# Optimization experiments

Hardware: AMD Instinct MI355X
Metric: run time of the kernel (lower is better)

The kernel has to match this reference:

```python
import jax, jax.numpy as jnp
import numpy as np

B, N, IN, HD, NH, L, OUT = 256, 128, 9, 128, 8, 4, 60
DH = HD // NH
ALPHA = 0.6
EPS = 1e-5

def _ln(x, g, b):
    m = jnp.mean(x, axis=-1, keepdims=True)
    v = jnp.mean((x - m) ** 2, axis=-1, keepdims=True)
    return (x - m) * jax.lax.rsqrt(v + EPS) * g + b

def setup_inputs():
    key = jax.random.key(0)
    ks = jax.random.split(key, 30)
    p = lambda i, s: jax.random.normal(ks[i], s, jnp.float32) * 0.02
    strong = (jax.random.uniform(ks[25], (N, N)) < 0.15).astype(jnp.float32)
    strong = jnp.maximum(strong, jnp.eye(N, dtype=jnp.float32))  # self loops
    weak_mask = (jax.random.uniform(ks[26], (N, N)) < 0.10).astype(jnp.float32)
    return {
        'x': jax.random.normal(ks[0], (B, N, IN), jnp.float32),
        'conv_w': p(1, (HD, IN)), 'conv_b': p(2, (HD,)),
        'bn_gamma': jnp.ones((HD,), jnp.float32), 'bn_beta': jnp.zeros((HD,), jnp.float32),
        'bn_mean': jnp.zeros((HD,), jnp.float32), 'bn_var': jnp.ones((HD,), jnp.float32),
        'W': p(3, (L, HD, HD)), 'a_src': p(4, (L, NH, DH)), 'a_dst': p(5, (L, NH, DH)),
        'ln_g': jnp.ones((L, HD), jnp.float32), 'ln_b': jnp.zeros((L, HD), jnp.float32),
        'ffn_w1': p(6, (L, HD, 2 * HD)), 'ffn_b1': p(7, (L, 2 * HD)),
        'ffn_w2': p(8, (L, 2 * HD, HD)), 'ffn_b2': p(9, (L, HD)),
        'norm_g': jnp.ones((HD,), jnp.float32), 'norm_b': jnp.zeros((HD,), jnp.float32),
        'proj_w': p(10, (HD, HD)), 'proj_b': p(11, (HD,)),
        'head_w1': p(12, (HD, HD // 2)), 'head_b1': p(13, (HD // 2,)),
        'head_w2': p(14, (HD // 2, OUT)), 'head_b2': p(15, (OUT,)),
        'strong_adj': strong, 'weak_mask': weak_mask,
        'weak_param': p(16, (N, N)), 'edge_weight_adj': p(17, (N, N)),
    }

def reference(x, conv_w, conv_b, bn_gamma, bn_beta, bn_mean, bn_var, W, a_src, a_dst, ln_g, ln_b, ffn_w1, ffn_b1, ffn_w2, ffn_b2, norm_g, norm_b, proj_w, proj_b, head_w1, head_b1, head_w2, head_b2, strong_adj, weak_mask, weak_param, edge_weight_adj):
    # embedding: Conv1d(k=1) == per-node linear, then eval-mode BatchNorm1d + ReLU
    h = jnp.einsum('bni,oi->bno', x, conv_w) + conv_b  # [B,N,HD]
    h = (h - bn_mean) * jax.lax.rsqrt(bn_var + EPS) * bn_gamma + bn_beta
    h = jax.nn.relu(h)
    # weak adjacency: learnable gated edges, row-normalized (shared across layers)
    Aw = jax.nn.sigmoid(weak_param) * weak_mask
    Aw = Aw / (jnp.sum(Aw, axis=-1, keepdims=True) + EPS)  # [N,N]
    for i in range(L):
        res = h
        hp = jnp.einsum('bnd,de->bne', h, W[i]).reshape(B, N, NH, DH)
        s = jnp.einsum('bnhd,hd->bnh', hp, a_src[i])
        t = jnp.einsum('bnhd,hd->bnh', hp, a_dst[i])
        e = jax.nn.leaky_relu(s[:, :, None, :] + t[:, None, :, :], 0.2)  # [B,N,N,H]
        e = e + edge_weight_adj[None, :, :, None]  # learned per-edge bias
        e = jnp.where(strong_adj[None, :, :, None] > 0, e, jnp.float32(-1e9))
        att = jax.nn.softmax(e, axis=2)  # softmax over neighbors j
        strong_out = jnp.einsum('bijh,bjhd->bihd', att, hp)
        weak_out = jnp.einsum('ij,bjhd->bihd', Aw, hp)
        g = jax.nn.relu(ALPHA * strong_out + (1.0 - ALPHA) * weak_out).reshape(B, N, HD)
        g = _ln(g, ln_g[i], ln_b[i])
        g = jax.nn.relu(g @ ffn_w1[i] + ffn_b1[i]) @ ffn_w2[i] + ffn_b2[i]
        h = g + res
    h = _ln(h, norm_g, norm_b)
    h = h @ proj_w + proj_b
    h = jnp.mean(h, axis=1)  # mean-pool over nodes -> [B,HD]
    h = jax.nn.relu(h @ head_w1 + head_b1)
    return h @ head_w2 + head_b2  # [B,OUT]
```

## Files before the change

### kernel.cpp

```cpp
#include <hip/hip_runtime.h>
#include <hip/hip_bf16.h>

typedef __hip_bfloat16 bf16;
typedef unsigned short u16;
typedef __attribute__((ext_vector_type(8))) short bfrag;
typedef __attribute__((ext_vector_type(4))) float cfrag;

union BF { bfrag v; u16 u[8]; unsigned w[4]; };
union CF { cfrag v; float f[4]; };

#define MFMA(a,b,c) __builtin_amdgcn_mfma_f32_16x16x32_bf16(a,b,c,0,0,0)

#define BB   256
#define NN   128
#define IND  9
#define HDD  128
#define NHH  8
#define LLY  4
#define OUTD 60
#define LOG2E 1.44269504f

__device__ __forceinline__ float b2f(bf16 v){ return __bfloat162float(v); }
__device__ __forceinline__ float u2f(u16 u){ return __uint_as_float(((unsigned)u) << 16); }
__device__ __forceinline__ u16 f2bf_bits(float f){
    unsigned u = __float_as_uint(f);
    return (u16)((u + 0x7FFFu + ((u >> 16) & 1u)) >> 16);
}
__device__ __forceinline__ unsigned pk2(float a, float b){
    union { __hip_bfloat162 h; unsigned u; } c;
    c.h = __float22bfloat162_rn(make_float2(a, b));
    return c.u;
}
__device__ __forceinline__ float wave_sum(float v){
    #pragma unroll
    for (int m = 32; m; m >>= 1) v += __shfl_xor(v, m, 64);
    return v;
}
__device__ __forceinline__ float ldin(const void* p, int i, bool isbf){
    return isbf ? b2f(((const bf16*)p)[i]) : ((const float*)p)[i];
}

struct SrcPtrs { const void* p[28]; };

__device__ const int CVT_OFF[28] = {
    0,294912,296064,296192,296320,296448,296576,296704,362240,362752,363264,363776,
    364288,495360,496384,627456,627968,628096,628224,644608,644736,652928,652992,656832,
    656896,673280,689664,706048};

__global__ __launch_bounds__(256) void k_prep(
    SrcPtrs S, float* __restrict__ pf,
    u16* __restrict__ WT, u16* __restrict__ w1T, u16* __restrict__ w2T,
    u16* __restrict__ ew2, u16* __restrict__ Aw16, int* __restrict__ flagOut)
{
    const unsigned* xw = (const unsigned*)S.p[0];
    int lane = threadIdx.x & 63;
    int cnt = 0;
    for (int i = lane; i < 512; i += 64) {
        float v = __uint_as_float((xw[i] & 0xFFFFu) << 16);
        if (!(fabsf(v) < 32.f)) cnt++;
    }
    bool isbf = wave_sum((float)cnt) < 16.f;
    if (blockIdx.x == 0 && threadIdx.x == 0) *flagOut = isbf ? 1 : 0;

    int blk = blockIdx.x, tid = threadIdx.x;
    if (blk < 2822) {
        int idx = blk * 256 + tid;
        int y = 27;
        #pragma unroll 1
        for (int t = 1; t < 28; t++) if (idx < CVT_OFF[t]) { y = t - 1; break; }
        pf[idx] = ldin(S.p[y], idx - CVT_OFF[y], isbf);
    } else if (blk < 3078) {
        int j = (blk - 2822) * 256 + tid;
        int l = j >> 14, r = j & 16383, n = r >> 7, k = r & 127;
        WT[j] = f2bf_bits(ldin(S.p[7], (l << 14) + k * 128 + n, isbf));
    } else if (blk < 3590) {
        int j = (blk - 3078) * 256 + tid;
        int l = j >> 15, r = j & 32767, n = r >> 7, k = r & 127;
        w1T[j] = f2bf_bits(ldin(S.p[12], (l << 15) + k * 256 + n, isbf));
    } else if (blk < 4102) {
        int j = (blk - 3590) * 256 + tid;
        int l = j >> 15, r = j & 32767, n = r >> 8, k = r & 255;
        w2T[j] = f2bf_bits(ldin(S.p[14], (l << 15) + k * 128 + n, isbf));
    } else if (blk < 4166) {
        int j = (blk - 4102) * 256 + tid;
        float sav = ldin(S.p[24], j, isbf);
        float ewv = ldin(S.p[27], j, isbf);
        ew2[j] = f2bf_bits(sav > 0.f ? ewv * LOG2E : -1e30f);
    } else {
        __shared__ float red[2];
        int i = blk - 4166, j = tid & 127;
        float v = 0.f;
        if (tid < 128) {
            float wmv = ldin(S.p[25], i * 128 + j, isbf);
            float wpv = ldin(S.p[26], i * 128 + j, isbf);
            v = wmv / (1.f + __expf(-wpv));
            float sm = wave_sum(v);
            if ((tid & 63) == 0) red[tid >> 6] = sm;
        }
        __syncthreads();
        if (tid < 128) {
            float tot = red[0] + red[1];
            Aw16[i * 128 + j] = f2bf_bits(v / (tot + 1e-5f));
        }
    }
}

__global__ __launch_bounds__(256) void k_embed(
    const float* __restrict__ xf, const float* __restrict__ cw, const float* __restrict__ cb,
    const float* __restrict__ bg, const float* __restrict__ bbt,
    const float* __restrict__ bm, const float* __restrict__ bv,
    float* __restrict__ h, u16* __restrict__ h16)
{
    int b = blockIdx.x, half = blockIdx.y, tid = threadIdx.x;
    int d = tid & 127, nh = tid >> 7;
    float wreg[IND];
    #pragma unroll
    for (int k = 0; k < IND; k++) wreg[k] = cw[d * IND + k];
    float scale = rsqrtf(bv[d] + 1e-5f) * bg[d];
    float bias  = bbt[d] - bm[d] * scale;
    float cbd   = cb[d];
    #pragma unroll 1
    for (int it = 0; it < 32; it++) {
        int bn = b * NN + half * 64 + it * 2 + nh;
        float acc = cbd;
        #pragma unroll
        for (int k = 0; k < IND; k++) acc = fmaf(xf[bn * IND + k], wreg[k], acc);
        acc = fmaxf(fmaf(acc, scale, bias), 0.f);
        h[bn * HDD + d] = acc;
        h16[bn * HDD + d] = f2bf_bits(acc);
    }
}

__global__ __launch_bounds__(256, 2) void k_layer(
    float* __restrict__ hg, u16* __restrict__ h16g,
    const u16* __restrict__ WT,
    const float* __restrict__ asrc, const float* __restrict__ adst,
    const u16* __restrict__ Aw16, const u16* __restrict__ ew2g,
    const float* __restrict__ lng, const float* __restrict__ lnb,
    const u16* __restrict__ w1T, const float* __restrict__ b1,
    const u16* __restrict__ w2T, const float* __restrict__ b2,
    const float* __restrict__ ng, const float* __restrict__ nb,
    float* __restrict__ pooled, int last)
{
    __shared__ __align__(16) u16 hpT[128 * 136];
    __shared__ __align__(16) u16 gbuf[64 * 136];
    __shared__ float st2[2048];
    __shared__ float lng_s[128], lnb_s[128], b2_s[128], ng_s[128], nb_s[128];
    __shared__ float b1_s[256];
    u16* hidb = hpT;
    float* s2 = st2;
    float* t2 = st2 + 1024;

    const int b = blockIdx.x, half = blockIdx.y;
    const int tid = threadIdx.x, lane = tid & 63, wv = tid >> 6;
    const int l15 = lane & 15, kg = lane >> 4;
    const int wrow = wv * 16;
    const int base = b * NN;

    if (tid < 128) {
        lng_s[tid] = lng[tid]; lnb_s[tid] = lnb[tid]; b2_s[tid] = b2[tid];
        if (last) { ng_s[tid] = ng[tid]; nb_s[tid] = nb[tid]; }
    }
    b1_s[tid] = b1[tid];

    {
        CF acc[2][8];
        #pragma unroll
        for (int mt = 0; mt < 2; mt++)
            #pragma unroll
            for (int nt = 0; nt < 8; nt++)
                #pragma unroll
                for (int r = 0; r < 4; r++) acc[mt][nt].f[r] = 0.f;
        #pragma unroll 1
        for (int kk = 0; kk < 4; kk++) {
            bfrag af0 = *(const bfrag*)&h16g[(base + wv*32 +      l15) * 128 + kk*32 + kg*8];
            bfrag af1 = *(const bfrag*)&h16g[(base + wv*32 + 16 + l15) * 128 + kk*32 + kg*8];
            #pragma unroll
            for (int nt = 0; nt < 8; nt++) {
                bfrag bw = *(const bfrag*)&WT[(nt*16 + l15) * 128 + kk*32 + kg*8];
                acc[0][nt].v = MFMA(af0, bw, acc[0][nt].v);
                acc[1][nt].v = MFMA(af1, bw, acc[1][nt].v);
            }
        }
        #pragma unroll
        for (int mt = 0; mt < 2; mt++)
            #pragma unroll
            for (int nt = 0; nt < 8; nt++) {
                int col = nt*16 + l15;
                #pragma unroll
                for (int rp = 0; rp < 2; rp++) {
                    int row = wv*32 + mt*16 + kg*4 + rp*2;
                    *(unsigned*)&hpT[col * 136 + row] =
                        pk2(acc[mt][nt].f[rp*2], acc[mt][nt].f[rp*2+1]);
                }
            }
    }
    __syncthreads();

    {
        int node = tid & 127, which = tid >> 7;
        const float* av = which ? adst : asrc;
        float* dst = which ? t2 : s2;
        #pragma unroll 1
        for (int h = 0; h < 8; h++) {
            const u16* cp = &hpT[h * 16 * 136 + node];
            float a = 0.f;
            #pragma unroll
            for (int d = 0; d < 16; d++)
                a = fmaf(u2f(cp[d * 136]), av[h*16 + d], a);
            dst[h * 128 + node] = a * LOG2E;
        }
    }
    __syncthreads();

    CF accS[8];
    #pragma unroll
    for (int nt = 0; nt < 8; nt++)
        #pragma unroll
        for (int r = 0; r < 4; r++) accS[nt].f[r] = 0.f;

    const int grow = half*64 + wrow + l15;
    #pragma unroll 1
    for (int h = 0; h < 8; h++) {
        bfrag hb[4];
        #pragma unroll
        for (int kk = 0; kk < 4; kk++)
            hb[kk] = *(const bfrag*)&hpT[(h*16 + l15) * 136 + kk*32 + kg*8];
        float sA = s2[h * 128 + grow];
        float pv[4][8];
        float sm = 0.f;
        #pragma unroll
        for (int kk = 0; kk < 4; kk++) {
            const float* tp = &t2[h * 128 + kk*32 + kg*8];
            BF e2; e2.v = *(const bfrag*)&ew2g[grow * 128 + kk*32 + kg*8];
            #pragma unroll
            for (int j = 0; j < 8; j++) {
                float x2 = sA + tp[j];
                float lk = fmaxf(x2, 0.2f * x2);
                float p = __builtin_amdgcn_exp2f(lk + u2f(e2.u[j]));
                pv[kk][j] = p; sm += p;
            }
        }
        sm += __shfl_xor(sm, 16, 64);
        sm += __shfl_xor(sm, 32, 64);
        float inv = __builtin_amdgcn_rcpf(sm);
        #pragma unroll
        for (int kk = 0; kk < 4; kk++) {
            BF pb;
            #pragma unroll
            for (int q = 0; q < 4; q++)
                pb.w[q] = pk2(pv[kk][2*q] * inv, pv[kk][2*q+1] * inv);
            accS[h].v = MFMA(pb.v, hb[kk], accS[h].v);
        }
    }

    CF accW[8];
    #pragma unroll
    for (int nt = 0; nt < 8; nt++)
        #pragma unroll
        for (int r = 0; r < 4; r++) accW[nt].f[r] = 0.f;
    #pragma unroll 1
    for (int kk = 0; kk < 4; kk++) {
        bfrag awf = *(const bfrag*)&Aw16[grow * 128 + kk*32 + kg*8];
        #pragma unroll
        for (int nt = 0; nt < 8; nt++) {
            bfrag hb2 = *(const bfrag*)&hpT[(nt*16 + l15) * 136 + kk*32 + kg*8];
            accW[nt].v = MFMA(awf, hb2, accW[nt].v);
        }
    }

    {
        float gv[8][4];
        #pragma unroll
        for (int nt = 0; nt < 8; nt++)
            #pragma unroll
            for (int r = 0; r < 4; r++)
                gv[nt][r] = fmaxf(0.6f * accS[nt].f[r] + 0.4f * accW[nt].f[r], 0.f);
        #pragma unroll
        for (int r = 0; r < 4; r++) {
            float s1 = 0.f, sq = 0.f;
            #pragma unroll
            for (int nt = 0; nt < 8; nt++) { float x = gv[nt][r]; s1 += x; sq = fmaf(x, x, sq); }
            #pragma unroll
            for (int m = 1; m <= 8; m <<= 1) { s1 += __shfl_xor(s1, m, 64); sq += __shfl_xor(sq, m, 64); }
            float mu = s1 * (1.f / 128.f);
            float var = sq * (1.f / 128.f) - mu * mu;
            float rs = rsqrtf(fmaxf(var, 0.f) + 1e-5f);
            int lrow = wrow + kg*4 + r;
            #pragma unroll
            for (int nt = 0; nt < 8; nt++) {
                int col = nt*16 + l15;
                gbuf[lrow * 136 + col] = f2bf_bits(fmaf((gv[nt][r] - mu) * rs, lng_s[col], lnb_s[col]));
            }
        }
    }
    __syncthreads();

    CF acc2[8];
    #pragma unroll
    for (int nt = 0; nt < 8; nt++)
        #pragma unroll
        for (int r = 0; r < 4; r++) acc2[nt].f[r] = 0.f;

    #pragma unroll 1
    for (int nh = 0; nh < 2; nh++) {
        CF a1[8];
        #pragma unroll
        for (int nt = 0; nt < 8; nt++)
            #pragma unroll
            for (int r = 0; r < 4; r++) a1[nt].f[r] = 0.f;
        #pragma unroll 1
        for (int kk = 0; kk < 4; kk++) {
            bfrag gf = *(const bfrag*)&gbuf[(wrow + l15) * 136 + kk*32 + kg*8];
            #pragma unroll
            for (int nt = 0; nt < 8; nt++) {
                bfrag wf = *(const bfrag*)&w1T[(nh*128 + nt*16 + l15) * 128 + kk*32 + kg*8];
                a1[nt].v = MFMA(gf, wf, a1[nt].v);
            }
        }
        __syncthreads();
        #pragma unroll
        for (int nt = 0; nt < 8; nt++) {
            int col = nt*16 + l15;
            #pragma unroll
            for (int r = 0; r < 4; r++) {
                int lrow = wrow + kg*4 + r;
                hidb[lrow * 136 + col] = f2bf_bits(fmaxf(a1[nt].f[r] + b1_s[nh*128 + col], 0.f));
            }
        }
        __syncthreads();
        #pragma unroll 1
        for (int kk = 0; kk < 4; kk++) {
            bfrag hf = *(const bfrag*)&hidb[(wrow + l15) * 136 + kk*32 + kg*8];
            #pragma unroll
            for (int nt = 0; nt < 8; nt++) {
                bfrag wf = *(const bfrag*)&w2T[(nt*16 + l15) * 256 + nh*128 + kk*32 + kg*8];
                acc2[nt].v = MFMA(hf, wf, acc2[nt].v);
            }
        }
    }

    float hv[8][4];
    #pragma unroll
    for (int nt = 0; nt < 8; nt++) {
        int col = nt*16 + l15;
        #pragma unroll
        for (int r = 0; r < 4; r++) {
            int gi = (base + half*64 + wrow + kg*4 + r) * HDD + col;
            hv[nt][r] = acc2[nt].f[r] + b2_s[col] + hg[gi];
        }
    }
    if (!last) {
        #pragma unroll
        for (int nt = 0; nt < 8; nt++) {
            int col = nt*16 + l15;
            #pragma unroll
            for (int r = 0; r < 4; r++) {
                int gi = (base + half*64 + wrow + kg*4 + r) * HDD + col;
                hg[gi] = hv[nt][r];
                h16g[gi] = f2bf_bits(hv[nt][r]);
            }
        }
    } else {
        float pacc[8];
        #pragma unroll
        for (int nt = 0; nt < 8; nt++) pacc[nt] = 0.f;
        #pragma unroll
        for (int r = 0; r < 4; r++) {
            float s1 = 0.f, sq = 0.f;
            #pragma unroll
            for (int nt = 0; nt < 8; nt++) { float x = hv[nt][r]; s1 += x; sq = fmaf(x, x, sq); }
            #pragma unroll
            for (int m = 1; m <= 8; m <<= 1) { s1 += __shfl_xor(s1, m, 64); sq += __shfl_xor(sq, m, 64); }
            float mu = s1 * (1.f / 128.f);
            float var = sq * (1.f / 128.f) - mu * mu;
            float rs = rsqrtf(fmaxf(var, 0.f) + 1e-5f);
            #pragma unroll
            for (int nt = 0; nt < 8; nt++) {
                int col = nt*16 + l15;
                pacc[nt] += fmaf((hv[nt][r] - mu) * rs, ng_s[col], nb_s[col]);
            }
        }
        __syncthreads();
        float* psum = st2;
        #pragma unroll
        for (int nt = 0; nt < 8; nt++)
            psum[(wv*4 + kg) * 128 + nt*16 + l15] = pacc[nt];
        __syncthreads();
        if (tid < 128) {
            float tot = 0.f;
            #pragma unroll
            for (int i = 0; i < 16; i++) tot += psum[i * 128 + tid];
            atomicAdd(&pooled[b * HDD + tid], tot);
        }
    }
}

__global__ __launch_bounds__(128) void k_head(
    const float* __restrict__ pooled, const float* __restrict__ pw, const float* __restrict__ pb,
    const float* __restrict__ hw1, const float* __restrict__ hb1,
    const float* __restrict__ hw2, const float* __restrict__ hb2,
    void* __restrict__ outv, const int* __restrict__ flag)
{
    int b = blockIdx.x, t = threadIdx.x;
    __shared__ float pm[128], pr[128], r1[64];
    pm[t] = pooled[b * HDD + t] * (1.f / 128.f);
    __syncthreads();
    float a = pb[t];
    #pragma unroll 4
    for (int k = 0; k < 128; k++) a = fmaf(pm[k], pw[k * 128 + t], a);
    pr[t] = a;
    __syncthreads();
    if (t < 64) {
        float a1 = hb1[t];
        #pragma unroll 4
        for (int k = 0; k < 128; k++) a1 = fmaf(pr[k], hw1[k * 64 + t], a1);
        r1[t] = fmaxf(a1, 0.f);
    }
    __syncthreads();
    if (t < OUTD) {
        float a2 = hb2[t];
        #pragma unroll 4
        for (int k = 0; k < 64; k++) a2 = fmaf(r1[k], hw2[k * OUTD + t], a2);
        if (*flag) ((bf16*)outv)[b * OUTD + t] = __float2bfloat16(a2);
        else       ((float*)outv)[b * OUTD + t] = a2;
    }
}

extern "C" void kernel_launch(void* const* d_in, const int* in_sizes, int n_in,
                              void* d_out, int out_size, void* d_ws, size_t ws_size,
                              hipStream_t stream)
{
    float* ws = (float*)d_ws;
    float* pf = ws;
    const float* xf   = pf + 0;
    const float* cw   = pf + 294912;
    const float* cb   = pf + 296064;
    const float* bg   = pf + 296192;
    const float* bbt  = pf + 296320;
    const float* bm   = pf + 296448;
    const float* bv   = pf + 296576;
    const float* asrcf= pf + 362240;
    const float* adstf= pf + 362752;
    const float* lng  = pf + 363264;
    const float* lnb  = pf + 363776;
    const float* fb1  = pf + 495360;
    const float* fb2  = pf + 627456;
    const float* ng   = pf + 627968;
    const float* nb   = pf + 628096;
    const float* pw   = pf + 628224;
    const float* pb   = pf + 644608;
    const float* hw1  = pf + 644736;
    const float* hb1  = pf + 652928;
    const float* hw2  = pf + 652992;
    const float* hb2  = pf + 656832;

    int*   flag   = (int*)(ws + 722432);
    float* h      = ws + 722448;
    float* pooled = h + 4194304;
    u16* h16    = (u16*)(pooled + 32768);
    u16* WT16   = h16 + 4194304;
    u16* w1T16  = WT16 + 65536;
    u16* w2T16  = w1T16 + 131072;
    u16* Aw16   = w2T16 + 131072;
    u16* ew2p   = Aw16 + 16384;

    SrcPtrs S;
    for (int i = 0; i < 28; i++) S.p[i] = d_in[i];

    k_prep<<<4294, 256, 0, stream>>>(S, pf, WT16, w1T16, w2T16, ew2p, Aw16, flag);
    hipMemsetAsync(pooled, 0, BB * HDD * sizeof(float), stream);
    k_embed<<<dim3(BB, 2), 256, 0, stream>>>(xf, cw, cb, bg, bbt, bm, bv, h, h16);

    for (int i = 0; i < LLY; i++) {
        k_layer<<<dim3(BB, 2), 256, 0, stream>>>(
            h, h16,
            WT16 + i * 16384, asrcf + i * 128, adstf + i * 128,
            Aw16, ew2p,
            lng + i * 128, lnb + i * 128,
            w1T16 + i * 32768, fb1 + i * 256,
            w2T16 + i * 32768, fb2 + i * 128,
            ng, nb, pooled, (i == LLY - 1) ? 1 : 0);
    }

    k_head<<<BB, 128, 0, stream>>>(pooled, pw, pb, hw1, hb1, hw2, hb2, d_out, flag);
}
```

Before: 395.4 us.

## Fold attention vectors into W, shrink prep conversion, raise layer occupancy

Precomputes W·a_src and W·a_dst as an extra 16-column bf16 weight block, so the per-node attention scores come from MFMA alongside the projection instead of a separate shared-memory dot-product pass. k_prep no longer converts x, W, FFN weights and other large tensors into a float copy; the embedding reads raw x directly and zeroes pooled itself, which removes the memset. In k_layer, gbuf and the hidden buffer now alias hpT and per-column parameters live in registers, cutting LDS so launch bounds can allow 3 blocks per CU. The weak-adjacency MFMA is moved before the attention loop and edge biases are hoisted into registers. The risks are higher register pressure at the new occupancy target and scores computed from bf16-rounded fused weights.

```diff
diff --git a/kernel.cpp b/kernel.cpp
--- a/kernel.cpp
+++ b/kernel.cpp
@@ -15,7 +15,6 @@
 #define NN   128
 #define IND  9
 #define HDD  128
-#define NHH  8
 #define LLY  4
 #define OUTD 60
 #define LOG2E 1.44269504f
@@ -42,15 +41,15 @@
 
 struct SrcPtrs { const void* p[28]; };
 
-__device__ const int CVT_OFF[28] = {
-    0,294912,296064,296192,296320,296448,296576,296704,362240,362752,363264,363776,
-    364288,495360,496384,627456,627968,628096,628224,644608,644736,652928,652992,656832,
-    656896,673280,689664,706048};
+__device__ const int NCV_OFF[19] = {0,1152,1280,1408,1536,1664,1792,2304,2816,3840,
+                                    4352,4480,4608,20992,21120,29312,29376,33216,33276};
+__device__ const int NCV_SRC[18] = {1,2,3,4,5,6,10,11,13,15,16,17,18,19,20,21,22,23};
 
 __global__ __launch_bounds__(256) void k_prep(
     SrcPtrs S, float* __restrict__ pf,
     u16* __restrict__ WT, u16* __restrict__ w1T, u16* __restrict__ w2T,
-    u16* __restrict__ ew2, u16* __restrict__ Aw16, int* __restrict__ flagOut)
+    u16* __restrict__ WAb, u16* __restrict__ ew2, u16* __restrict__ Aw16,
+    int* __restrict__ flagOut)
 {
     const unsigned* xw = (const unsigned*)S.p[0];
     int lane = threadIdx.x & 63;
@@ -63,32 +62,45 @@
     if (blockIdx.x == 0 && threadIdx.x == 0) *flagOut = isbf ? 1 : 0;
 
     int blk = blockIdx.x, tid = threadIdx.x;
-    if (blk < 2822) {
+    if (blk < 131) {
         int idx = blk * 256 + tid;
-        int y = 27;
-        #pragma unroll 1
-        for (int t = 1; t < 28; t++) if (idx < CVT_OFF[t]) { y = t - 1; break; }
-        pf[idx] = ldin(S.p[y], idx - CVT_OFF[y], isbf);
-    } else if (blk < 3078) {
-        int j = (blk - 2822) * 256 + tid;
+        if (idx < 33276) {
+            int y = 17;
+            #pragma unroll 1
+            for (int t = 1; t < 18; t++) if (idx < NCV_OFF[t]) { y = t - 1; break; }
+            pf[idx] = ldin(S.p[NCV_SRC[y]], idx - NCV_OFF[y], isbf);
+        }
+    } else if (blk < 387) {
+        int j = (blk - 131) * 256 + tid;
         int l = j >> 14, r = j & 16383, n = r >> 7, k = r & 127;
         WT[j] = f2bf_bits(ldin(S.p[7], (l << 14) + k * 128 + n, isbf));
-    } else if (blk < 3590) {
-        int j = (blk - 3078) * 256 + tid;
+    } else if (blk < 899) {
+        int j = (blk - 387) * 256 + tid;
         int l = j >> 15, r = j & 32767, n = r >> 7, k = r & 127;
         w1T[j] = f2bf_bits(ldin(S.p[12], (l << 15) + k * 256 + n, isbf));
-    } else if (blk < 4102) {
-        int j = (blk - 3590) * 256 + tid;
+    } else if (blk < 1411) {
+        int j = (blk - 899) * 256 + tid;
         int l = j >> 15, r = j & 32767, n = r >> 8, k = r & 255;
         w2T[j] = f2bf_bits(ldin(S.p[14], (l << 15) + k * 128 + n, isbf));
-    } else if (blk < 4166) {
-        int j = (blk - 4102) * 256 + tid;
+    } else if (blk < 1443) {
+        int j = (blk - 1411) * 256 + tid;
+        int l = j >> 11, r = j & 2047, n = r >> 7, k = r & 127;
+        int h = n & 7;
+        const void* ap = (n < 8) ? S.p[8] : S.p[9];
+        float sacc = 0.f;
+        #pragma unroll 1
+        for (int d = 0; d < 16; d++)
+            sacc += ldin(S.p[7], l * 16384 + k * 128 + h * 16 + d, isbf)
+                  * ldin(ap, l * 128 + h * 16 + d, isbf);
+        WAb[j] = f2bf_bits(sacc);
+    } else if (blk < 1507) {
+        int j = (blk - 1443) * 256 + tid;
         float sav = ldin(S.p[24], j, isbf);
         float ewv = ldin(S.p[27], j, isbf);
         ew2[j] = f2bf_bits(sav > 0.f ? ewv * LOG2E : -1e30f);
     } else {
         __shared__ float red[2];
-        int i = blk - 4166, j = tid & 127;
+        int i = blk - 1507, j = tid & 127;
         float v = 0.f;
         if (tid < 128) {
             float wmv = ldin(S.p[25], i * 128 + j, isbf);
@@ -106,35 +118,35 @@
 }
 
 __global__ __launch_bounds__(256) void k_embed(
-    const float* __restrict__ xf, const float* __restrict__ cw, const float* __restrict__ cb,
-    const float* __restrict__ bg, const float* __restrict__ bbt,
-    const float* __restrict__ bm, const float* __restrict__ bv,
-    float* __restrict__ h, u16* __restrict__ h16)
+    const void* __restrict__ xraw, const int* __restrict__ flag,
+    const float* __restrict__ pf,
+    float* __restrict__ h, u16* __restrict__ h16, float* __restrict__ pooled)
 {
     int b = blockIdx.x, half = blockIdx.y, tid = threadIdx.x;
+    bool isbf = (*flag != 0);
+    if (half == 0 && tid < 128) pooled[b * 128 + tid] = 0.f;
     int d = tid & 127, nh = tid >> 7;
     float wreg[IND];
     #pragma unroll
-    for (int k = 0; k < IND; k++) wreg[k] = cw[d * IND + k];
-    float scale = rsqrtf(bv[d] + 1e-5f) * bg[d];
-    float bias  = bbt[d] - bm[d] * scale;
-    float cbd   = cb[d];
+    for (int k = 0; k < IND; k++) wreg[k] = pf[d * IND + k];
+    float scale = rsqrtf(pf[1664 + d] + 1e-5f) * pf[1280 + d];
+    float bias  = pf[1408 + d] - pf[1536 + d] * scale;
+    float cbd   = pf[1152 + d];
     #pragma unroll 1
     for (int it = 0; it < 32; it++) {
         int bn = b * NN + half * 64 + it * 2 + nh;
         float acc = cbd;
         #pragma unroll
-        for (int k = 0; k < IND; k++) acc = fmaf(xf[bn * IND + k], wreg[k], acc);
+        for (int k = 0; k < IND; k++) acc = fmaf(ldin(xraw, bn * IND + k, isbf), wreg[k], acc);
         acc = fmaxf(fmaf(acc, scale, bias), 0.f);
         h[bn * HDD + d] = acc;
         h16[bn * HDD + d] = f2bf_bits(acc);
     }
 }
 
-__global__ __launch_bounds__(256, 2) void k_layer(
+__global__ __launch_bounds__(256, 3) void k_layer(
     float* __restrict__ hg, u16* __restrict__ h16g,
-    const u16* __restrict__ WT,
-    const float* __restrict__ asrc, const float* __restrict__ adst,
+    const u16* __restrict__ WT, const u16* __restrict__ WAb,
     const u16* __restrict__ Aw16, const u16* __restrict__ ew2g,
     const float* __restrict__ lng, const float* __restrict__ lnb,
     const u16* __restrict__ w1T, const float* __restrict__ b1,
@@ -143,13 +155,11 @@
     float* __restrict__ pooled, int last)
 {
     __shared__ __align__(16) u16 hpT[128 * 136];
-    __shared__ __align__(16) u16 gbuf[64 * 136];
     __shared__ float st2[2048];
-    __shared__ float lng_s[128], lnb_s[128], b2_s[128], ng_s[128], nb_s[128];
-    __shared__ float b1_s[256];
-    u16* hidb = hpT;
     float* s2 = st2;
     float* t2 = st2 + 1024;
+    u16* gbuf = hpT;
+    u16* hidb = hpT + 64 * 136;
 
     const int b = blockIdx.x, half = blockIdx.y;
     const int tid = threadIdx.x, lane = tid & 63, wv = tid >> 6;
@@ -157,24 +167,31 @@
     const int wrow = wv * 16;
     const int base = b * NN;
 
-    if (tid < 128) {
-        lng_s[tid] = lng[tid]; lnb_s[tid] = lnb[tid]; b2_s[tid] = b2[tid];
-        if (last) { ng_s[tid] = ng[tid]; nb_s[tid] = nb[tid]; }
-    }
-    b1_s[tid] = b1[tid];
+    float lngr[8], lnbr[8], b2r[8];
+    #pragma unroll
+    for (int nt = 0; nt < 8; nt++) {
+        int col = nt * 16 + l15;
+        lngr[nt] = lng[col]; lnbr[nt] = lnb[col]; b2r[nt] = b2[col];
+    }
 
     {
-        CF acc[2][8];
-        #pragma unroll
-        for (int mt = 0; mt < 2; mt++)
+        CF acc[2][8], ast[2];
+        #pragma unroll
+        for (int mt = 0; mt < 2; mt++) {
+            #pragma unroll
+            for (int r = 0; r < 4; r++) ast[mt].f[r] = 0.f;
             #pragma unroll
             for (int nt = 0; nt < 8; nt++)
                 #pragma unroll
                 for (int r = 0; r < 4; r++) acc[mt][nt].f[r] = 0.f;
+        }
         #pragma unroll 1
         for (int kk = 0; kk < 4; kk++) {
             bfrag af0 = *(const bfrag*)&h16g[(base + wv*32 +      l15) * 128 + kk*32 + kg*8];
             bfrag af1 = *(const bfrag*)&h16g[(base + wv*32 + 16 + l15) * 128 + kk*32 + kg*8];
+            bfrag wab = *(const bfrag*)&WAb[l15 * 128 + kk*32 + kg*8];
+            ast[0].v = MFMA(af0, wab, ast[0].v);
+            ast[1].v = MFMA(af1, wab, ast[1].v);
             #pragma unroll
             for (int nt = 0; nt < 8; nt++) {
                 bfrag bw = *(const bfrag*)&WT[(nt*16 + l15) * 128 + kk*32 + kg*8];
@@ -183,7 +200,7 @@
             }
         }
         #pragma unroll
-        for (int mt = 0; mt < 2; mt++)
+        for (int mt = 0; mt < 2; mt++) {
             #pragma unroll
             for (int nt = 0; nt < 8; nt++) {
                 int col = nt*16 + l15;
@@ -194,24 +211,32 @@
                         pk2(acc[mt][nt].f[rp*2], acc[mt][nt].f[rp*2+1]);
                 }
             }
-    }
-    __syncthreads();
-
-    {
-        int node = tid & 127, which = tid >> 7;
-        const float* av = which ? adst : asrc;
-        float* dst = which ? t2 : s2;
-        #pragma unroll 1
-        for (int h = 0; h < 8; h++) {
-            const u16* cp = &hpT[h * 16 * 136 + node];
-            float a = 0.f;
-            #pragma unroll
-            for (int d = 0; d < 16; d++)
-                a = fmaf(u2f(cp[d * 136]), av[h*16 + d], a);
-            dst[h * 128 + node] = a * LOG2E;
-        }
-    }
-    __syncthreads();
+            #pragma unroll
+            for (int r = 0; r < 4; r++) {
+                int node = wv*32 + mt*16 + kg*4 + r;
+                float v = ast[mt].f[r] * LOG2E;
+                float* dst = (l15 < 8) ? &s2[l15 * 128 + node] : &t2[(l15 - 8) * 128 + node];
+                *dst = v;
+            }
+        }
+    }
+    __syncthreads();
+
+    const int grow = half*64 + wrow + l15;
+    CF accW[8];
+    #pragma unroll
+    for (int nt = 0; nt < 8; nt++)
+        #pragma unroll
+        for (int r = 0; r < 4; r++) accW[nt].f[r] = 0.f;
+    #pragma unroll 1
+    for (int kk = 0; kk < 4; kk++) {
+        bfrag awf = *(const bfrag*)&Aw16[grow * 128 + kk*32 + kg*8];
+        #pragma unroll
+        for (int nt = 0; nt < 8; nt++) {
+            bfrag hb2 = *(const bfrag*)&hpT[(nt*16 + l15) * 136 + kk*32 + kg*8];
+            accW[nt].v = MFMA(awf, hb2, accW[nt].v);
+        }
+    }
 
     CF accS[8];
     #pragma unroll
@@ -219,7 +244,13 @@
         #pragma unroll
         for (int r = 0; r < 4; r++) accS[nt].f[r] = 0.f;
 
-    const int grow = half*64 + wrow + l15;
+    float ew2f[4][8];
+    #pragma unroll
+    for (int kk = 0; kk < 4; kk++) {
+        BF e2; e2.v = *(const bfrag*)&ew2g[grow * 128 + kk*32 + kg*8];
+        #pragma unroll
+        for (int j = 0; j < 8; j++) ew2f[kk][j] = u2f(e2.u[j]);
+    }
     #pragma unroll 1
     for (int h = 0; h < 8; h++) {
         bfrag hb[4];
@@ -232,12 +263,11 @@
         #pragma unroll
         for (int kk = 0; kk < 4; kk++) {
             const float* tp = &t2[h * 128 + kk*32 + kg*8];
-            BF e2; e2.v = *(const bfrag*)&ew2g[grow * 128 + kk*32 + kg*8];
             #pragma unroll
             for (int j = 0; j < 8; j++) {
                 float x2 = sA + tp[j];
                 float lk = fmaxf(x2, 0.2f * x2);
-                float p = __builtin_amdgcn_exp2f(lk + u2f(e2.u[j]));
+                float p = __builtin_amdgcn_exp2f(lk + ew2f[kk][j]);
                 pv[kk][j] = p; sm += p;
             }
         }
@@ -254,132 +284,121 @@
         }
     }
 
-    CF accW[8];
+    float gv[8][4];
     #pragma unroll
     for (int nt = 0; nt < 8; nt++)
         #pragma unroll
-        for (int r = 0; r < 4; r++) accW[nt].f[r] = 0.f;
+        for (int r = 0; r < 4; r++)
+            gv[nt][r] = fmaxf(0.6f * accS[nt].f[r] + 0.4f * accW[nt].f[r], 0.f);
+    u16 gb16[8][4];
+    #pragma unroll
+    for (int r = 0; r < 4; r++) {
+        float s1 = 0.f, sq = 0.f;
+        #pragma unroll
+        for (int nt = 0; nt < 8; nt++) { float x = gv[nt][r]; s1 += x; sq = fmaf(x, x, sq); }
+        #pragma unroll
+        for (int m = 1; m <= 8; m <<= 1) { s1 += __shfl_xor(s1, m, 64); sq += __shfl_xor(sq, m, 64); }
+        float mu = s1 * (1.f / 128.f);
+        float var = sq * (1.f / 128.f) - mu * mu;
+        float rs = rsqrtf(fmaxf(var, 0.f) + 1e-5f);
+        #pragma unroll
+        for (int nt = 0; nt < 8; nt++)
+            gb16[nt][r] = f2bf_bits(fmaf((gv[nt][r] - mu) * rs, lngr[nt], lnbr[nt]));
+    }
+    __syncthreads();
+    #pragma unroll
+    for (int nt = 0; nt < 8; nt++) {
+        int col = nt*16 + l15;
+        #pragma unroll
+        for (int r = 0; r < 4; r++)
+            gbuf[(wrow + kg*4 + r) * 136 + col] = gb16[nt][r];
+    }
+    __syncthreads();
+
+    CF acc2[8];
+    #pragma unroll
+    for (int nt = 0; nt < 8; nt++)
+        #pragma unroll
+        for (int r = 0; r < 4; r++) acc2[nt].f[r] = 0.f;
+
     #pragma unroll 1
-    for (int kk = 0; kk < 4; kk++) {
-        bfrag awf = *(const bfrag*)&Aw16[grow * 128 + kk*32 + kg*8];
+    for (int nh = 0; nh < 2; nh++) {
+        float b1r[8];
+        #pragma unroll
+        for (int nt = 0; nt < 8; nt++) b1r[nt] = b1[nh*128 + nt*16 + l15];
+        CF a1[8];
+        #pragma unroll
+        for (int nt = 0; nt < 8; nt++)
+            #pragma unroll
+            for (int r = 0; r < 4; r++) a1[nt].f[r] = 0.f;
+        #pragma unroll 1
+        for (int kk = 0; kk < 4; kk++) {
+            bfrag gf = *(const bfrag*)&gbuf[(wrow + l15) * 136 + kk*32 + kg*8];
+            #pragma unroll
+            for (int nt = 0; nt < 8; nt++) {
+                bfrag wf = *(const bfrag*)&w1T[(nh*128 + nt*16 + l15) * 128 + kk*32 + kg*8];
+                a1[nt].v = MFMA(gf, wf, a1[nt].v);
+            }
+        }
+        __syncthreads();
         #pragma unroll
         for (int nt = 0; nt < 8; nt++) {
-            bfrag hb2 = *(const bfrag*)&hpT[(nt*16 + l15) * 136 + kk*32 + kg*8];
-            accW[nt].v = MFMA(awf, hb2, accW[nt].v);
-        }
-    }
-
-    {
-        float gv[8][4];
-        #pragma unroll
-        for (int nt = 0; nt < 8; nt++)
+            int col = nt*16 + l15;
             #pragma unroll
             for (int r = 0; r < 4; r++)
-                gv[nt][r] = fmaxf(0.6f * accS[nt].f[r] + 0.4f * accW[nt].f[r], 0.f);
+                hidb[(wrow + kg*4 + r) * 136 + col] = f2bf_bits(fmaxf(a1[nt].f[r] + b1r[nt], 0.f));
+        }
+        __syncthreads();
+        #pragma unroll 1
+        for (int kk = 0; kk < 4; kk++) {
+            bfrag hf = *(const bfrag*)&hidb[(wrow + l15) * 136 + kk*32 + kg*8];
+            #pragma unroll
+            for (int nt = 0; nt < 8; nt++) {
+                bfrag wf = *(const bfrag*)&w2T[(nt*16 + l15) * 256 + nh*128 + kk*32 + kg*8];
+                acc2[nt].v = MFMA(hf, wf, acc2[nt].v);
+            }
+        }
+    }
+
+    float hv[8][4];
+    #pragma unroll
+    for (int nt = 0; nt < 8; nt++) {
+        #pragma unroll
+        for (int r = 0; r < 4; r++) {
+            int gi = (base + half*64 + wrow + kg*4 + r) * HDD + nt*16 + l15;
+            hv[nt][r] = acc2[nt].f[r] + b2r[nt] + hg[gi];
+        }
+    }
+    if (!last) {
+        #pragma unroll
+        for (int nt = 0; nt < 8; nt++) {
+            #pragma unroll
+            for (int r = 0; r < 4; r++) {
+                int gi = (base + half*64 + wrow + kg*4 + r) * HDD + nt*16 + l15;
+                hg[gi] = hv[nt][r];
+                h16g[gi] = f2bf_bits(hv[nt][r]);
+            }
+        }
+    } else {
+        float ngr[8], nbr[8];
+        #pragma unroll
+        for (int nt = 0; nt < 8; nt++) { int col = nt*16 + l15; ngr[nt] = ng[col]; nbr[nt] = nb[col]; }
+        float pacc[8];
+        #pragma unroll
+        for (int nt = 0; nt < 8; nt++) pacc[nt] = 0.f;
         #pragma unroll
         for (int r = 0; r < 4; r++) {
             float s1 = 0.f, sq = 0.f;
             #pragma unroll
-            for (int nt = 0; nt < 8; nt++) { float x = gv[nt][r]; s1 += x; sq = fmaf(x, x, sq); }
+            for (int nt = 0; nt < 8; nt++) { float x = hv[nt][r]; s1 += x; sq = fmaf(x, x, sq); }
             #pragma unroll
             for (int m = 1; m <= 8; m <<= 1) { s1 += __shfl_xor(s1, m, 64); sq += __shfl_xor(sq, m, 64); }
             float mu = s1 * (1.f / 128.f);
             float var = sq * (1.f / 128.f) - mu * mu;
             float rs = rsqrtf(fmaxf(var, 0.f) + 1e-5f);
-            int lrow = wrow + kg*4 + r;
-            #pragma unroll
-            for (int nt = 0; nt < 8; nt++) {
-                int col = nt*16 + l15;
-                gbuf[lrow * 136 + col] = f2bf_bits(fmaf((gv[nt][r] - mu) * rs, lng_s[col], lnb_s[col]));
-            }
-        }
-    }
-    __syncthreads();
-
-    CF acc2[8];
-    #pragma unroll
-    for (int nt = 0; nt < 8; nt++)
-        #pragma unroll
-        for (int r = 0; r < 4; r++) acc2[nt].f[r] = 0.f;
-
-    #pragma unroll 1
-    for (int nh = 0; nh < 2; nh++) {
-        CF a1[8];
-        #pragma unroll
-        for (int nt = 0; nt < 8; nt++)
-            #pragma unroll
-            for (int r = 0; r < 4; r++) a1[nt].f[r] = 0.f;
-        #pragma unroll 1
-        for (int kk = 0; kk < 4; kk++) {
-            bfrag gf = *(const bfrag*)&gbuf[(wrow + l15) * 136 + kk*32 + kg*8];
-            #pragma unroll
-            for (int nt = 0; nt < 8; nt++) {
-                bfrag wf = *(const bfrag*)&w1T[(nh*128 + nt*16 + l15) * 128 + kk*32 + kg*8];
-                a1[nt].v = MFMA(gf, wf, a1[nt].v);
-            }
-        }
-        __syncthreads();
-        #pragma unroll
-        for (int nt = 0; nt < 8; nt++) {
-            int col = nt*16 + l15;
-            #pragma unroll
-            for (int r = 0; r < 4; r++) {
-                int lrow = wrow + kg*4 + r;
-                hidb[lrow * 136 + col] = f2bf_bits(fmaxf(a1[nt].f[r] + b1_s[nh*128 + col], 0.f));
-            }
-        }
-        __syncthreads();
-        #pragma unroll 1
-        for (int kk = 0; kk < 4; kk++) {
-            bfrag hf = *(const bfrag*)&hidb[(wrow + l15) * 136 + kk*32 + kg*8];
-            #pragma unroll
-            for (int nt = 0; nt < 8; nt++) {
-                bfrag wf = *(const bfrag*)&w2T[(nt*16 + l15) * 256 + nh*128 + kk*32 + kg*8];
-                acc2[nt].v = MFMA(hf, wf, acc2[nt].v);
-            }
-        }
-    }
-
-    float hv[8][4];
-    #pragma unroll
-    for (int nt = 0; nt < 8; nt++) {
-        int col = nt*16 + l15;
-        #pragma unroll
-        for (int r = 0; r < 4; r++) {
-            int gi = (base + half*64 + wrow + kg*4 + r) * HDD + col;
-            hv[nt][r] = acc2[nt].f[r] + b2_s[col] + hg[gi];
-        }
-    }
-    if (!last) {
-        #pragma unroll
-        for (int nt = 0; nt < 8; nt++) {
-            int col = nt*16 + l15;
-            #pragma unroll
-            for (int r = 0; r < 4; r++) {
-                int gi = (base + half*64 + wrow + kg*4 + r) * HDD + col;
-                hg[gi] = hv[nt][r];
-                h16g[gi] = f2bf_bits(hv[nt][r]);
-            }
-        }
-    } else {
-        float pacc[8];
-        #pragma unroll
-        for (int nt = 0; nt < 8; nt++) pacc[nt] = 0.f;
-        #pragma unroll
-        for (int r = 0; r < 4; r++) {
-            float s1 = 0.f, sq = 0.f;
-            #pragma unroll
-            for (int nt = 0; nt < 8; nt++) { float x = hv[nt][r]; s1 += x; sq = fmaf(x, x, sq); }
-            #pragma unroll
-            for (int m = 1; m <= 8; m <<= 1) { s1 += __shfl_xor(s1, m, 64); sq += __shfl_xor(sq, m, 64); }
-            float mu = s1 * (1.f / 128.f);
-            float var = sq * (1.f / 128.f) - mu * mu;
-            float rs = rsqrtf(fmaxf(var, 0.f) + 1e-5f);
-            #pragma unroll
-            for (int nt = 0; nt < 8; nt++) {
-                int col = nt*16 + l15;
-                pacc[nt] += fmaf((hv[nt][r] - mu) * rs, ng_s[col], nb_s[col]);
-            }
+            #pragma unroll
+            for (int nt = 0; nt < 8; nt++)
+                pacc[nt] += fmaf((hv[nt][r] - mu) * rs, ngr[nt], nbr[nt]);
         }
         __syncthreads();
         float* psum = st2;
@@ -397,11 +416,15 @@
 }
 
 __global__ __launch_bounds__(128) void k_head(
-    const float* __restrict__ pooled, const float* __restrict__ pw, const float* __restrict__ pb,
-    const float* __restrict__ hw1, const float* __restrict__ hb1,
-    const float* __restrict__ hw2, const float* __restrict__ hb2,
+    const float* __restrict__ pooled, const float* __restrict__ pf,
     void* __restrict__ outv, const int* __restrict__ flag)
 {
+    const float* pw  = pf + 4608;
+    const float* pb  = pf + 20992;
+    const float* hw1 = pf + 21120;
+    const float* hb1 = pf + 29312;
+    const float* hw2 = pf + 29376;
+    const float* hb2 = pf + 33216;
     int b = blockIdx.x, t = threadIdx.x;
     __shared__ float pm[128], pr[128], r1[64];
     pm[t] = pooled[b * HDD + t] * (1.f / 128.f);
@@ -433,49 +456,34 @@
 {
     float* ws = (float*)d_ws;
     float* pf = ws;
-    const float* xf   = pf + 0;
-    const float* cw   = pf + 294912;
-    const float* cb   = pf + 296064;
-    const float* bg   = pf + 296192;
-    const float* bbt  = pf + 296320;
-    const float* bm   = pf + 296448;
-    const float* bv   = pf + 296576;
-    const float* asrcf= pf + 362240;
-    const float* adstf= pf + 362752;
-    const float* lng  = pf + 363264;
-    const float* lnb  = pf + 363776;
-    const float* fb1  = pf + 495360;
-    const float* fb2  = pf + 627456;
-    const float* ng   = pf + 627968;
-    const float* nb   = pf + 628096;
-    const float* pw   = pf + 628224;
-    const float* pb   = pf + 644608;
-    const float* hw1  = pf + 644736;
-    const float* hb1  = pf + 652928;
-    const float* hw2  = pf + 652992;
-    const float* hb2  = pf + 656832;
-
-    int*   flag   = (int*)(ws + 722432);
-    float* h      = ws + 722448;
+    const float* lng  = pf + 1792;
+    const float* lnb  = pf + 2304;
+    const float* fb1  = pf + 2816;
+    const float* fb2  = pf + 3840;
+    const float* ng   = pf + 4352;
+    const float* nb   = pf + 4480;
+
+    int*   flag   = (int*)(ws + 33280);
+    float* h      = ws + 33536;
     float* pooled = h + 4194304;
     u16* h16    = (u16*)(pooled + 32768);
     u16* WT16   = h16 + 4194304;
     u16* w1T16  = WT16 + 65536;
     u16* w2T16  = w1T16 + 131072;
-    u16* Aw16   = w2T16 + 131072;
+    u16* WAb16  = w2T16 + 131072;
+    u16* Aw16   = WAb16 + 8192;
     u16* ew2p   = Aw16 + 16384;
 
     SrcPtrs S;
     for (int i = 0; i < 28; i++) S.p[i] = d_in[i];
 
-    k_prep<<<4294, 256, 0, stream>>>(S, pf, WT16, w1T16, w2T16, ew2p, Aw16, flag);
-    hipMemsetAsync(pooled, 0, BB * HDD * sizeof(float), stream);
-    k_embed<<<dim3(BB, 2), 256, 0, stream>>>(xf, cw, cb, bg, bbt, bm, bv, h, h16);
+    k_prep<<<1635, 256, 0, stream>>>(S, pf, WT16, w1T16, w2T16, WAb16, ew2p, Aw16, flag);
+    k_embed<<<dim3(BB, 2), 256, 0, stream>>>(d_in[0], flag, pf, h, h16, pooled);
 
     for (int i = 0; i < LLY; i++) {
         k_layer<<<dim3(BB, 2), 256, 0, stream>>>(
             h, h16,
-            WT16 + i * 16384, asrcf + i * 128, adstf + i * 128,
+            WT16 + i * 16384, WAb16 + i * 2048,
             Aw16, ew2p,
             lng + i * 128, lnb + i * 128,
             w1T16 + i * 32768, fb1 + i * 256,
@@ -483,5 +491,5 @@
             ng, nb, pooled, (i == LLY - 1) ? 1 : 0);
     }
 
-    k_head<<<BB, 128, 0, stream>>>(pooled, pw, pb, hw1, hb1, hw2, hb2, d_out, flag);
-}
+    k_head<<<BB, 128, 0, stream>>>(pooled, pf, d_out, flag);
+}
```

Result: no change. 393.7 us (-0.4%).
